# Kernel tuning notes

Hardware: AMD Instinct MI355X
Metric: run time of the kernel (lower is better)

Reference implementation:

```python
import jax, jax.numpy as jnp
import numpy as np
from jax import lax

DN = ('NCHW', 'OIHW', 'NCHW')
NUM_CODES = 8192


def _conv(x, w, b):
    # Conv2d(k=4, s=2, p=1)
    y = lax.conv_general_dilated(x, w, (2, 2), ((1, 1), (1, 1)), dimension_numbers=DN)
    return y + b[None, :, None, None]


def _convT(x, w, b):
    # ConvTranspose2d(k=4, s=2, p=1) as lhs-dilated conv; kernel already in equivalent OIHW layout
    y = lax.conv_general_dilated(x, w, (1, 1), ((2, 2), (2, 2)), lhs_dilation=(2, 2), dimension_numbers=DN)
    return y + b[None, :, None, None]


def _aff(x, s, b):
    # eval-mode BatchNorm folded to per-channel affine
    return x * s[None, :, None, None] + b[None, :, None, None]


def _forward(x, ew1, eb1, bn1s, bn1b, ew2, eb2, bn2s, bn2b, ew3, eb3, bn3s, bn3b, ew4, eb4, embed, cluster_size, dw1, db1, dbn1s, dbn1b, dw2, db2, dbn2s, dbn2b, dw3, db3, dbn3s, dbn3b, dw4, db4):
    sg = lax.stop_gradient
    embed = sg(embed)          # codebook is a torch buffer -> no grad
    cluster_size = sg(cluster_size)
    relu = jax.nn.relu
    # ---- Encoder: 4 stride-2 convs ----
    h = relu(_aff(_conv(x, ew1, eb1), bn1s, bn1b))
    h = relu(_aff(_conv(h, ew2, eb2), bn2s, bn2b))
    h = relu(_aff(_conv(h, ew3, eb3), bn3s, bn3b))
    z = _conv(h, ew4, eb4)                       # [B, D, G, G]
    zt = jnp.transpose(z, (0, 2, 3, 1))          # [B, G, G, D]
    D = zt.shape[-1]
    flat = zt.reshape(-1, D)                     # [N, D]
    N = flat.shape[0]
    # ---- VQ: pairwise squared distance + argmin codebook lookup ----
    dist = (flat * flat).sum(1, keepdims=True) - 2.0 * (flat @ embed.T) + (embed * embed).sum(1)[None, :]
    soft = jax.nn.softmax(-dist, axis=-1)        # temperature = 1.0
    codes = jnp.argmin(dist, axis=1)             # [N]
    zq = embed[codes]                            # [N, D]
    commitment_loss = jnp.mean((flat - sg(zq)) ** 2)
    codebook_loss = jnp.mean((zq - sg(flat)) ** 2)
    avg_soft = soft.mean(0)
    usage_entropy = -(avg_soft * jnp.log(avg_soft + 1e-10)).sum()
    diversity_loss = -usage_entropy / float(np.log(NUM_CODES))
    zq_st = flat + sg(zq - flat)                 # straight-through estimator
    zq_grid = jnp.transpose(zq_st.reshape(zt.shape), (0, 3, 1, 2))  # [B, D, G, G]
    # ---- Decoder: 4 stride-2 transposed convs ----
    h = relu(_aff(_convT(zq_grid, dw1, db1), dbn1s, dbn1b))
    h = relu(_aff(_convT(h, dw2, db2), dbn2s, dbn2b))
    h = relu(_aff(_convT(h, dw3, db3), dbn3s, dbn3b))
    recon = jax.nn.sigmoid(_convT(h, dw4, db4))
    recon_loss = jnp.mean((recon - x) ** 2)
    # ---- usage stats (no-grad in torch) ----
    hard_avg = jnp.zeros(NUM_CODES, flat.dtype).at[codes].add(1.0) / N
    perplexity = jnp.exp(-(hard_avg * jnp.log(hard_avg + 1e-10)).sum())
    active_codes = (cluster_size > 1).sum()
    codes_grid = codes.reshape(zt.shape[:-1])
    return (recon, recon_loss, codes_grid, zq_grid, commitment_loss, codebook_loss, diversity_loss, usage_entropy, perplexity, active_codes)


def setup_inputs() -> dict:
    keys = iter(jax.random.split(jax.random.key(0), 64))
    def randn(shape, s=1.0):
        return jax.random.normal(next(keys), shape, jnp.float32) * s
    def randu(shape):
        return jax.random.uniform(next(keys), shape, dtype=jnp.float32)
    B, H = 32, 256
    return {
        'x': randu((B, 1, H, H)),
        'ew1': randn((64, 1, 4, 4), 0.25), 'eb1': randn((64,), 0.1),
        'bn1s': randu((64,)), 'bn1b': randn((64,), 0.1),
        'ew2': randn((64, 64, 4, 4), 0.03), 'eb2': randn((64,), 0.1),
        'bn2s': randu((64,)), 'bn2b': randn((64,), 0.1),
        'ew3': randn((128, 64, 4, 4), 0.03), 'eb3': randn((128,), 0.1),
        'bn3s': randu((128,)), 'bn3b': randn((128,), 0.1),
        'ew4': randn((64, 128, 4, 4), 0.02), 'eb4': randn((64,), 0.1),
        'embed': randn((8192, 64), 0.5),
        'cluster_size': jnp.ones((8192,), jnp.float32),
        'dw1': randn((128, 64, 4, 4), 0.03), 'db1': randn((128,), 0.1),
        'dbn1s': randu((128,)), 'dbn1b': randn((128,), 0.1),
        'dw2': randn((64, 128, 4, 4), 0.02), 'db2': randn((64,), 0.1),
        'dbn2s': randu((64,)), 'dbn2b': randn((64,), 0.1),
        'dw3': randn((64, 64, 4, 4), 0.03), 'db3': randn((64,), 0.1),
        'dbn3s': randu((64,)), 'dbn3b': randn((64,), 0.1),
        'dw4': randn((1, 64, 4, 4), 0.03), 'db4': randn((1,), 0.1),
    }


def reference(x, ew1, eb1, bn1s, bn1b, ew2, eb2, bn2s, bn2b, ew3, eb3, bn3s, bn3b, ew4, eb4, embed, cluster_size, dw1, db1, dbn1s, dbn1b, dw2, db2, dbn2s, dbn2b, dw3, db3, dbn3s, dbn3b, dw4, db4):
    return _forward(x, ew1, eb1, bn1s, bn1b, ew2, eb2, bn2s, bn2b, ew3, eb3, bn3s, bn3b, ew4, eb4, embed, cluster_size, dw1, db1, dbn1s, dbn1b, dw2, db2, dbn2s, dbn2b, dw3, db3, dbn3s, dbn3b, dw4, db4)
```

## Files before the change

kernel.cpp:

```cpp
#include <hip/hip_runtime.h>
#include <cstdint>
#include <cstddef>


#define DEVI __device__ __forceinline__

typedef short  short8 __attribute__((ext_vector_type(8)));
typedef __bf16 bf16x8 __attribute__((ext_vector_type(8)));
typedef float  f32x16 __attribute__((ext_vector_type(16)));

DEVI f32x16 MFMA(bf16x8 a, bf16x8 b, f32x16 c){
  return __builtin_amdgcn_mfma_f32_32x32x16_bf16(a, b, c, 0, 0, 0);
}

DEVI ushort f2bf(float f){
  unsigned u = __float_as_uint(f);
  unsigned r = (u + 0x7FFFu + ((u >> 16) & 1u)) >> 16;
  return (ushort)r;
}
DEVI float bf2f(ushort h){ return __uint_as_float(((unsigned)h) << 16); }

union U8 { short8 s; bf16x8 b; };
DEVI bf16x8 ldg8u(const ushort* p){
  U8 u; u.s = *(const short8*)p; return u.b;
}

DEVI float wred64(float v){
  #pragma unroll
  for (int off=32; off>0; off>>=1) v += __shfl_down(v, off, 64);
  return v;
}

#define O_RECON     0
#define O_RLOSS     2097152
#define O_CODES     2097153
#define O_ZQ        2105345
#define O_COMMIT    2629633
#define O_CB        2629634
#define O_DIV       2629635
#define O_UE        2629636
#define O_PERP      2629637
#define O_ACT       2629638

#define WS_R1       0ull
#define A3H_OFF     0ull
#define A3M_OFF     8912896ull
#define A3L_OFF     17825792ull
#define PP_OFF      33554432ull
#define MT_OFF      37748736ull
#define PARTA_OFF   41943040ull
#define A2H_OFF     134217728ull
#define A2M_OFF     151519232ull
#define A2L_OFF     168820736ull
#define EH_OFF      134217728ull
#define EM_OFF      135266304ull
#define EL_OFF      136314880ull
#define FH_OFF      137363456ull
#define FM_OFF      138412032ull
#define FL_OFF      139460608ull
#define D2H_OFF     134217728ull
#define D2L_OFF     151519232ull
#define D1H_OFF     168820736ull
#define D1L_OFF     177733632ull
#define WS_FLAT     186646528ull
#define WS_ZQP      188743680ull
#define WS_WT       191102976ull
#define WT_E2       (WS_WT)
#define WT_E3       (WT_E2 + 393216ull)
#define WT_E4       (WT_E3 + 786432ull)
#define WT_D1       (WT_E4 + 786432ull)
#define WT_D2       (WT_D1 + 524288ull)
#define WT_D3       (WT_D2 + 524288ull)
#define WS_W4       (WT_D3 + 262144ull)
#define WS_STATS    (WS_W4 + 4096ull)
#define ST_RMP      (WS_STATS)
#define ST_CNT      (ST_RMP + 65536ull)
#define ST_AVGS     (ST_CNT + 32768ull)
#define ST_ROWZI    (ST_AVGS + 32768ull)
#define ST_CODESQ   (ST_ROWZI + 32768ull)
#define ST_LOSS     (ST_CODESQ + 32768ull)
#define ST_ROWM     (ST_LOSS + 32768ull)

DEVI void wsplit_body(int i, const float* src, ushort* dh, ushort* dm,
                      ushort* dl, int OC, int CIN, int isT, int three)
{
  if (i >= 16*OC*CIN) return;
  int cin = i % CIN; int t = i / CIN; int oc = t % OC; int tap = t / OC;
  int st;
  if (isT){
    int pq = tap>>2, ab = tap&3;
    int p = pq>>1, q = pq&1, a = ab>>1, b = ab&1;
    st = (p + 2*a)*4 + (q + 2*b);
  } else st = tap;
  float v = src[((size_t)oc*CIN + cin)*16 + st];
  ushort h = f2bf(v); float r = v - bf2f(h);
  if (three){
    ushort m = f2bf(r); float r2 = r - bf2f(m);
    dm[i] = m; dl[i] = f2bf(r2);
  } else {
    dl[i] = f2bf(r);
  }
  dh[i] = h;
}

DEVI void zpad_body(int i, unsigned* b0, unsigned* b1, unsigned* b2,
                    int rows, int Wp, int cwords)
{
  int total = rows*2*cwords;
  if (i >= total) return;
  int pos = i / cwords, cw = i % cwords;
  int row = pos >> 1, side = pos & 1;
  size_t w = ((size_t)row*Wp + (side ? (Wp-1) : 0))*cwords + cw;
  b0[w] = 0u;
  if (b1) b1[w] = 0u;
  if (b2) b2[w] = 0u;
}

__global__ __launch_bounds__(256) void k_prep(
    const float* __restrict__ ew2, const float* __restrict__ ew3,
    const float* __restrict__ ew4, const float* __restrict__ dw1,
    const float* __restrict__ dw2, const float* __restrict__ dw3,
    const float* __restrict__ dw4,
    ushort* wE2h, ushort* wE2m, ushort* wE2l,
    ushort* wE3h, ushort* wE3m, ushort* wE3l,
    ushort* wE4h, ushort* wE4m, ushort* wE4l,
    ushort* wD1h, ushort* wD1l, ushort* wD2h, ushort* wD2l,
    ushort* wD3h, ushort* wD3l, float* w4,
    unsigned* A2h, unsigned* A2m, unsigned* A2l,
    unsigned* zqPh, unsigned* zqPl,
    unsigned int* cnt, unsigned long long* rmp, float* loss)
{
  int b = blockIdx.x, tid = threadIdx.x;
  if (b < 32){
    int i = b*256 + tid;
    if (i < 8192){ cnt[i]=0u; rmp[i]=0xFFFFFFFFFFFFFFFFull; }
    if (i < 8) loss[i]=0.f;
  } else if (b < 288){
    wsplit_body((b-32)*256 + tid, ew2, wE2h, wE2m, wE2l, 64, 64, 0, 1);
  } else if (b < 800){
    wsplit_body((b-288)*256 + tid, ew3, wE3h, wE3m, wE3l, 128, 64, 0, 1);
  } else if (b < 1312){
    wsplit_body((b-800)*256 + tid, ew4, wE4h, wE4m, wE4l, 64, 128, 0, 1);
  } else if (b < 1824){
    wsplit_body((b-1312)*256 + tid, dw1, wD1h, nullptr, wD1l, 128, 64, 1, 0);
  } else if (b < 2336){
    wsplit_body((b-1824)*256 + tid, dw2, wD2h, nullptr, wD2l, 64, 128, 1, 0);
  } else if (b < 2592){
    wsplit_body((b-2336)*256 + tid, dw3, wD3h, nullptr, wD3l, 64, 64, 1, 0);
  } else if (b < 2596){
    int i = (b-2592)*256 + tid;
    if (i < 1024){
      int c = i & 63; int t16 = i >> 6;
      int pq = t16 >> 2, ab = t16 & 3;
      int p = pq>>1, q = pq&1, a = ab>>1, bb = ab&1;
      w4[i] = dw4[(size_t)c*16 + (p+2*a)*4 + (q+2*bb)];
    }
  } else if (b < 3108){
    zpad_body((b-2596)*256 + tid, A2h, A2m, A2l, 32*64, 66, 32);
  } else {
    zpad_body((b-3108)*256 + tid, zqPh, zqPl, nullptr, 32*16, 18, 32);
  }
}

__global__ __launch_bounds__(256) void k_zpadA3(unsigned* b0, unsigned* b1,
                                                unsigned* b2)
{
  zpad_body(blockIdx.x*256 + threadIdx.x, b0, b1, b2, 32*32, 34, 64);
}
__global__ __launch_bounds__(256) void k_zpadD(unsigned* d1h, unsigned* d1l,
                                               unsigned* d2h, unsigned* d2l)
{
  int b = blockIdx.x;
  if (b < 512) zpad_body(b*256 + threadIdx.x, d1h, d1l, nullptr, 32*32, 34, 64);
  else zpad_body((b-512)*256 + threadIdx.x, d2h, d2l, nullptr, 32*64, 66, 32);
}

__global__ __launch_bounds__(256) void k_esplit(
    const float* __restrict__ src, ushort* __restrict__ dh,
    ushort* __restrict__ dm, ushort* __restrict__ dl)
{
  int i = blockIdx.x*256 + threadIdx.x;
  float v = src[i];
  ushort h = f2bf(v); float r1 = v - bf2f(h);
  ushort m = f2bf(r1); float r2 = r1 - bf2f(m);
  dh[i] = h; dm[i] = m; dl[i] = f2bf(r2);
}

__global__ __launch_bounds__(256) void enc_conv1(
    const float* __restrict__ x, const float* __restrict__ w,
    const float* __restrict__ cb_, const float* __restrict__ bns,
    const float* __restrict__ bnb, float* __restrict__ out)
{
  __shared__ __align__(16) float sIn[34][36];
  __shared__ __align__(16) float sW[64][16];
  int b = blockIdx.x;
  int t = b & 63, n = b >> 6;
  int ty = t >> 3, tx = t & 7;
  int oy0 = ty*16, ox0 = tx*16;
  int iy0 = 2*oy0 - 1, ix0 = 2*ox0 - 1;
  int tid = threadIdx.x;
  int spg = tid & 31, og = tid >> 5;
  int sy = spg >> 1, x0 = (spg & 1)*8;

  if (tid < 64){
    const float* wp = w + tid*16;
    *(float4*)&sW[tid][0]  = *(const float4*)(wp);
    *(float4*)&sW[tid][4]  = *(const float4*)(wp+4);
    *(float4*)&sW[tid][8]  = *(const float4*)(wp+8);
    *(float4*)&sW[tid][12] = *(const float4*)(wp+12);
  }
  for (int e = tid; e < 34*34; e += 256){
    int rr = e/34, cc = e%34;
    int iy = iy0+rr, ix = ix0+cc;
    float v = 0.f;
    if ((unsigned)iy < 256u && (unsigned)ix < 256u)
      v = x[(size_t)n*65536 + iy*256 + ix];
    sIn[rr][cc] = v;
  }
  __syncthreads();

  float acc[8][8];
  #pragma unroll
  for (int j=0;j<8;j++)
    #pragma unroll
    for (int xi=0;xi<8;xi++) acc[j][xi]=0.f;

  #pragma unroll
  for (int ky=0; ky<4; ky++){
    int riy = 2*sy + ky;
    float seg[20];
    #pragma unroll
    for (int i=0;i<5;i++){
      float4 v = *(const float4*)&sIn[riy][2*x0 + 4*i];
      seg[4*i+0]=v.x; seg[4*i+1]=v.y; seg[4*i+2]=v.z; seg[4*i+3]=v.w;
    }
    #pragma unroll
    for (int j=0;j<8;j++){
      float4 w4v = *(const float4*)&sW[og*8+j][ky*4];
      #pragma unroll
      for (int xi=0; xi<8; xi++){
        acc[j][xi] = fmaf(seg[2*xi+0], w4v.x,
                     fmaf(seg[2*xi+1], w4v.y,
                     fmaf(seg[2*xi+2], w4v.z,
                     fmaf(seg[2*xi+3], w4v.w, acc[j][xi]))));
      }
    }
  }

  float sc[8], sh[8];
  #pragma unroll
  for (int j=0;j<8;j++){
    int oc = og*8+j;
    sc[j] = bns[oc];
    sh[j] = fmaf(cb_[oc], sc[j], bnb[oc]);
  }
  int oy = oy0 + sy;
  #pragma unroll
  for (int xi=0; xi<8; xi++){
    int oxg = ox0 + x0 + xi;
    float* op = out + (((size_t)n*128 + oy)*128 + oxg)*64 + og*8;
    float4 q0, q1;
    q0.x = fmaxf(fmaf(acc[0][xi], sc[0], sh[0]), 0.f);
    q0.y = fmaxf(fmaf(acc[1][xi], sc[1], sh[1]), 0.f);
    q0.z = fmaxf(fmaf(acc[2][xi], sc[2], sh[2]), 0.f);
    q0.w = fmaxf(fmaf(acc[3][xi], sc[3], sh[3]), 0.f);
    q1.x = fmaxf(fmaf(acc[4][xi], sc[4], sh[4]), 0.f);
    q1.y = fmaxf(fmaf(acc[5][xi], sc[5], sh[5]), 0.f);
    q1.z = fmaxf(fmaf(acc[6][xi], sc[6], sh[6]), 0.f);
    q1.w = fmaxf(fmaf(acc[7][xi], sc[7], sh[7]), 0.f);
    *(float4*)op     = q0;
    *(float4*)(op+4) = q1;
  }
}

template<int CIN, int OC, int OUTW, int OUTH, int INW, int INH, bool XPAD,
         int INMODE, int OUTMODE>
__global__ __launch_bounds__(256) void enc_conv(
    const float* __restrict__ in,
    const ushort* __restrict__ aH, const ushort* __restrict__ aM,
    const ushort* __restrict__ aL,
    const ushort* __restrict__ wtH, const ushort* __restrict__ wtM,
    const ushort* __restrict__ wtL,
    const float* __restrict__ cb_, const float* __restrict__ bns,
    const float* __restrict__ bnb,
    float* __restrict__ outF,
    ushort* __restrict__ oH, ushort* __restrict__ oM, ushort* __restrict__ oL,
    int nOcg)
{
  constexpr int INWP  = (INMODE==1) ? (INW+2) : (XPAD ? (INW+2) : INW);
  constexpr int WP    = INW + 2;
  constexpr int NROWS = 64 / OUTW;
  constexpr int AELEM = NROWS * WP * CIN;
  constexpr int BCIN  = (CIN > 64) ? 64 : CIN;
  constexpr int BELEM = 64 * BCIN;
  constexpr int NCH   = CIN / BCIN;
  constexpr int NSTG  = 16 * NCH;
  constexpr int PFI   = BELEM / 8 / 256;
  constexpr int SCRSZ = (3*BELEM*2 > 64*68*4) ? 3*BELEM*2 : 64*68*4;

  __shared__ __align__(16) ushort sAh[AELEM], sAm[AELEM], sAl[AELEM];
  __shared__ __align__(16) char sScr[SCRSZ];
  ushort* sBh = (ushort*)sScr;
  ushort* sBm = sBh + BELEM;
  ushort* sBl = sBm + BELEM;
  float*  sC  = (float*)sScr;

  int b = blockIdx.x;
  int ocg = b % nOcg; b /= nOcg;
  int yb  = b % (OUTH/NROWS); b /= (OUTH/NROWS);
  int n = b;
  int oy0 = yb * NROWS, oc0 = ocg * 64;

  int tid = threadIdx.x;
  int l = tid & 63, wave = tid >> 6;
  int wm = wave >> 1, wn = wave & 1;
  int r = l & 31, kp = l >> 5;
  int idx = wm*32 + r;
  int oy_off = idx / OUTW, ox = idx % OUTW;

  int pfoc[PFI], pfc8[PFI];
  #pragma unroll
  for (int it=0; it<PFI; it++){
    int c = tid + it*256;
    pfoc[it] = c / (BCIN/8);
    pfc8[it] = (c % (BCIN/8)) * 8;
  }
  short8 pf0[PFI], pf1[PFI], pf2[PFI];
  {
    #pragma unroll
    for (int it=0; it<PFI; it++){
      size_t off = ((size_t)oc0 + pfoc[it])*CIN + pfc8[it];
      pf0[it] = *(const short8*)(wtH + off);
      pf1[it] = *(const short8*)(wtM + off);
      pf2[it] = *(const short8*)(wtL + off);
    }
  }

  f32x16 acc0, acc1, acc2, acc3;
  #pragma unroll
  for (int i=0;i<16;i++){ acc0[i]=0.f; acc1[i]=0.f; acc2[i]=0.f; acc3[i]=0.f; }

  const size_t nbase = (size_t)n * INH * INWP * CIN;
  int sidx = 0;

  for (int ky = 0; ky < 4; ky++){
    __syncthreads();
    for (int c = tid; c < AELEM/8; c += 256){
      int j  = c / (WP*CIN/8);
      int rm = c % (WP*CIN/8);
      int lx = rm / (CIN/8);
      int c8 = (rm % (CIN/8)) * 8;
      int iy = 2*(oy0 + j) - 1 + ky;
      bool ok = (unsigned)iy < (unsigned)INH;
      unsigned off = (unsigned)(((j*WP + lx)*CIN + c8)*2) ^ ((((unsigned)lx>>1)&15u)<<4);
      if constexpr (INMODE == 0){
        int gx = XPAD ? lx : (lx - 1);
        if (!XPAD) ok = ok && ((unsigned)gx < (unsigned)INW);
        float4 v0 = {0,0,0,0}, v1 = {0,0,0,0};
        if (ok){
          const float* s = in + nbase + ((size_t)iy*INWP + gx)*CIN + c8;
          v0 = *(const float4*)s; v1 = *(const float4*)(s+4);
        }
        float vv[8] = {v0.x,v0.y,v0.z,v0.w,v1.x,v1.y,v1.z,v1.w};
        short8 hh, mm, ll;
        #pragma unroll
        for (int e=0;e<8;e++){
          ushort h = f2bf(vv[e]); float r1 = vv[e] - bf2f(h);
          ushort m = f2bf(r1);    float r2 = r1 - bf2f(m);
          hh[e] = (short)h; mm[e] = (short)m; ll[e] = (short)f2bf(r2);
        }
        *(short8*)((char*)sAh + off) = hh;
        *(short8*)((char*)sAm + off) = mm;
        *(short8*)((char*)sAl + off) = ll;
      } else {
        short8 vh = {0,0,0,0,0,0,0,0}, vm = vh, vl = vh;
        if (ok){
          size_t s = nbase + ((size_t)iy*INWP + lx)*CIN + c8;
          vh = *(const short8*)(aH + s);
          vm = *(const short8*)(aM + s);
          vl = *(const short8*)(aL + s);
        }
        *(short8*)((char*)sAh + off) = vh;
        *(short8*)((char*)sAm + off) = vm;
        *(short8*)((char*)sAl + off) = vl;
      }
    }
    for (int kx = 0; kx < 4; kx++){
      for (int chi = 0; chi < NCH; chi++){
        int ch = chi * BCIN;
        __syncthreads();
        #pragma unroll
        for (int it=0; it<PFI; it++){
          unsigned off = (unsigned)((pfoc[it]*BCIN + pfc8[it])*2)
                         ^ (((unsigned)pfoc[it]&15u)<<4);
          *(short8*)((char*)sBh + off) = pf0[it];
          *(short8*)((char*)sBm + off) = pf1[it];
          *(short8*)((char*)sBl + off) = pf2[it];
        }
        __syncthreads();
        if (sidx + 1 < NSTG){
          int ns = sidx + 1;
          int ntap = ns / NCH, nchi = ns % NCH;
          #pragma unroll
          for (int it=0; it<PFI; it++){
            size_t off = ((size_t)ntap*OC + oc0 + pfoc[it])*CIN
                         + nchi*BCIN + pfc8[it];
            pf0[it] = *(const short8*)(wtH + off);
            pf1[it] = *(const short8*)(wtM + off);
            pf2[it] = *(const short8*)(wtL + off);
          }
        }
        sidx++;
        int lx = 2*ox + kx;
        unsigned asw  = ((((unsigned)lx>>1)&15u)<<4);
        unsigned alin = (unsigned)(((oy_off*WP + lx)*CIN)*2);
        int ocl = wn*32 + r;
        unsigned bsw  = (((unsigned)ocl&15u)<<4);
        unsigned blin = (unsigned)((ocl*BCIN)*2);
        #pragma unroll
        for (int ct = 0; ct < BCIN/16; ct++){
          unsigned kbA = (unsigned)((ch + ct*16 + kp*8)*2);
          unsigned kbB = (unsigned)((ct*16 + kp*8)*2);
          unsigned ao = (alin + kbA) ^ asw;
          unsigned bo = (blin + kbB) ^ bsw;
          bf16x8 ah = *(const bf16x8*)((char*)sAh + ao);
          bf16x8 am = *(const bf16x8*)((char*)sAm + ao);
          bf16x8 al = *(const bf16x8*)((char*)sAl + ao);
          bf16x8 bh = *(const bf16x8*)((char*)sBh + bo);
          bf16x8 bm = *(const bf16x8*)((char*)sBm + bo);
          bf16x8 bl = *(const bf16x8*)((char*)sBl + bo);
          acc0 = MFMA(ah, bh, acc0);
          acc1 = MFMA(ah, bm, acc1);
          acc2 = MFMA(am, bh, acc2);
          acc3 = MFMA(ah, bl, acc3);
          acc0 = MFMA(am, bm, acc0);
          acc1 = MFMA(al, bh, acc1);
        }
      }
    }
  }
  __syncthreads();
  #pragma unroll
  for (int q = 0; q < 16; q++){
    int rowt = (q&3) + 8*(q>>2) + 4*kp;
    sC[(wm*32 + rowt)*68 + wn*32 + r] = (acc0[q] + acc1[q]) + (acc2[q] + acc3[q]);
  }
  __syncthreads();
  {
    int m = tid >> 2, qq = tid & 3;
    int oc = oc0 + qq*16;
    int oyg = oy0 + m / OUTW;
    int oxg = m % OUTW;
    if constexpr (OUTMODE == 1){
      size_t row = (size_t)n*256 + oyg*16 + oxg;
      float* op = outF + row*64 + qq*16;
      size_t pb = row*64 + qq*16;
      short8 hv[2], mv[2], lv[2];
      #pragma unroll
      for (int i=0;i<16;i++){
        float v = sC[m*68 + qq*16 + i] + cb_[oc+i];
        op[i] = v;
        ushort h = f2bf(v); float r1 = v - bf2f(h);
        ushort mm = f2bf(r1); float r2 = r1 - bf2f(mm);
        hv[i>>3][i&7]=(short)h; mv[i>>3][i&7]=(short)mm; lv[i>>3][i&7]=(short)f2bf(r2);
      }
      *(short8*)(oH + pb) = hv[0]; *(short8*)(oH + pb + 8) = hv[1];
      *(short8*)(oM + pb) = mv[0]; *(short8*)(oM + pb + 8) = mv[1];
      *(short8*)(oL + pb) = lv[0]; *(short8*)(oL + pb + 8) = lv[1];
    } else {
      size_t pbase = (((size_t)n*OUTH + oyg)*(OUTW+2) + oxg + 1)*OC + oc;
      short8 hv[2], mv[2], lv[2];
      #pragma unroll
      for (int i=0;i<16;i++){
        float s1 = bns[oc+i];
        float s2 = fmaf(cb_[oc+i], s1, bnb[oc+i]);
        float v = fmaxf(fmaf(sC[m*68 + qq*16 + i], s1, s2), 0.f);
        ushort h = f2bf(v); float r1 = v - bf2f(h);
        ushort mm = f2bf(r1); float r2 = r1 - bf2f(mm);
        hv[i>>3][i&7]=(short)h; mv[i>>3][i&7]=(short)mm; lv[i>>3][i&7]=(short)f2bf(r2);
      }
      *(short8*)(oH + pbase)   = hv[0]; *(short8*)(oH + pbase+8) = hv[1];
      *(short8*)(oM + pbase)   = mv[0]; *(short8*)(oM + pbase+8) = mv[1];
      *(short8*)(oL + pbase)   = lv[0]; *(short8*)(oL + pbase+8) = lv[1];
    }
  }
}

__global__ __launch_bounds__(256) void k_codesq(const float* __restrict__ embed,
                                                float* __restrict__ codesq)
{
  int j = blockIdx.x*4 + (threadIdx.x>>6);
  int c = threadIdx.x & 63;
  float e = embed[(size_t)j*64 + c];
  float s = wred64(e*e);
  if (c==0) codesq[j] = s;
}

DEVI float rmp_minval(unsigned long long v){
  unsigned skey = (unsigned)(v >> 32);
  unsigned u = (skey & 0x80000000u) ? (skey ^ 0x80000000u) : ~skey;
  return __uint_as_float(u);
}

__global__ __launch_bounds__(256) void vq_min(
    const ushort* __restrict__ fH, const ushort* __restrict__ fM,
    const ushort* __restrict__ fL,
    const ushort* __restrict__ eH, const ushort* __restrict__ eM,
    const ushort* __restrict__ eL,
    const float* __restrict__ codesq,
    unsigned long long* __restrict__ rmp,
    float* __restrict__ Pp, float* __restrict__ Mt)
{
  __shared__ __align__(16) ushort sAh[128*64], sAm[128*64], sAl[128*64];
  int cblk = blockIdx.x & 63, fblk = blockIdx.x >> 6;
  int code0 = cblk*128, f0 = fblk*128;
  int tid = threadIdx.x, l = tid&63, wave = tid>>6;
  int wm = wave>>1, wn = wave&1, r = l&31, kp = l>>5;

  for (int c = tid; c < 1024; c += 256){
    int rr = c >> 3, c8 = (c & 7)*8;
    size_t s = (size_t)(code0+rr)*64 + c8;
    unsigned off = (unsigned)((rr*64 + c8)*2) ^ (((unsigned)rr&15u)<<4);
    *(short8*)((char*)sAh + off) = *(const short8*)(eH + s);
    *(short8*)((char*)sAm + off) = *(const short8*)(eM + s);
    *(short8*)((char*)sAl + off) = *(const short8*)(eL + s);
  }
  __syncthreads();

  f32x16 acc[2][2];
  #pragma unroll
  for (int mt=0;mt<2;mt++)
    #pragma unroll
    for (int nt=0;nt<2;nt++)
      #pragma unroll
      for (int i=0;i<16;i++) acc[mt][nt][i]=0.f;

  #pragma unroll
  for (int ks=0; ks<4; ks++){
    unsigned kb = (unsigned)((ks*16 + kp*8)*2);
    int ko = ks*16 + kp*8;
    bf16x8 Ah[2],Am[2],Al[2],Bh[2],Bm[2],Bl[2];
    #pragma unroll
    for (int mt=0;mt<2;mt++){
      int rowi = wm*64 + mt*32 + r;
      unsigned o = ((unsigned)(rowi*128) + kb) ^ (((unsigned)rowi&15u)<<4);
      Ah[mt] = *(const bf16x8*)((char*)sAh + o);
      Am[mt] = *(const bf16x8*)((char*)sAm + o);
      Al[mt] = *(const bf16x8*)((char*)sAl + o);
    }
    #pragma unroll
    for (int nt=0;nt<2;nt++){
      int coli = f0 + wn*64 + nt*32 + r;
      size_t bo = (size_t)coli*64 + ko;
      Bh[nt] = ldg8u(fH + bo);
      Bm[nt] = ldg8u(fM + bo);
      Bl[nt] = ldg8u(fL + bo);
    }
    #pragma unroll
    for (int mt=0;mt<2;mt++)
      #pragma unroll
      for (int nt=0;nt<2;nt++){
        acc[mt][nt] = MFMA(Ah[mt], Bh[nt], acc[mt][nt]);
        acc[mt][nt] = MFMA(Ah[mt], Bm[nt], acc[mt][nt]);
        acc[mt][nt] = MFMA(Am[mt], Bh[nt], acc[mt][nt]);
        acc[mt][nt] = MFMA(Ah[mt], Bl[nt], acc[mt][nt]);
        acc[mt][nt] = MFMA(Am[mt], Bm[nt], acc[mt][nt]);
        acc[mt][nt] = MFMA(Al[mt], Bh[nt], acc[mt][nt]);
      }
  }

  float cqv[2][16];
  #pragma unroll
  for (int mt=0; mt<2; mt++)
    #pragma unroll
    for (int g=0; g<4; g++){
      float4 cv = *(const float4*)(codesq + code0 + wm*64 + mt*32 + 8*g + 4*kp);
      cqv[mt][4*g+0]=cv.x; cqv[mt][4*g+1]=cv.y;
      cqv[mt][4*g+2]=cv.z; cqv[mt][4*g+3]=cv.w;
    }

  #pragma unroll
  for (int nt=0; nt<2; nt++){
    int col = f0 + wn*64 + nt*32 + r;
    unsigned long long kmin = 0xFFFFFFFFFFFFFFFFull;
    #pragma unroll
    for (int mt=0; mt<2; mt++)
      #pragma unroll
      for (int q=0; q<16; q++){
        float d = cqv[mt][q] - 2.f*acc[mt][nt][q];
        int code = code0 + wm*64 + mt*32 + (q&3) + 8*(q>>2) + 4*kp;
        unsigned u = __float_as_uint(d);
        unsigned sgn = (unsigned)((int)u >> 31);
        unsigned skey = u ^ (sgn | 0x80000000u);
        unsigned long long key = (((unsigned long long)skey)<<32) | (unsigned)code;
        if (key < kmin) kmin = key;
      }
    unsigned long long o2 = __shfl_xor(kmin, 32, 64);
    if (o2 < kmin) kmin = o2;
    float mloc = rmp_minval(kmin);
    float p = 0.f;
    #pragma unroll
    for (int mt=0; mt<2; mt++)
      #pragma unroll
      for (int q=0; q<16; q++){
        float d = cqv[mt][q] - 2.f*acc[mt][nt][q];
        p += __expf(mloc - d);
      }
    p += __shfl_xor(p, 32, 64);
    if (kp == 0){
      atomicMin(&rmp[col], kmin);
      size_t pidx = (size_t)col*128 + (size_t)cblk*2 + wm;
      Pp[pidx] = p;
      Mt[pidx] = mloc;
    }
  }
}

__global__ __launch_bounds__(256) void k_rowz2(
    const unsigned long long* __restrict__ rmp,
    const float* __restrict__ Pp, const float* __restrict__ Mt,
    float* __restrict__ rowzi, float* __restrict__ rowm)
{
  int row = blockIdx.x*256 + threadIdx.x;
  float mg = rmp_minval(rmp[row]);
  const float* pp = Pp + (size_t)row*128;
  const float* mt = Mt + (size_t)row*128;
  float z = 0.f;
  for (int t = 0; t < 128; t++)
    z = fmaf(__expf(mg - mt[t]), pp[t], z);
  rowzi[row] = 1.f / z;
  rowm[row] = mg;
}

__global__ __launch_bounds__(256) void vq_avg(
    const ushort* __restrict__ fH, const ushort* __restrict__ fM,
    const ushort* __restrict__ fL,
    const ushort* __restrict__ eH, const ushort* __restrict__ eM,
    const ushort* __restrict__ eL,
    const float* __restrict__ codesq,
    const float* __restrict__ rowm,
    const float* __restrict__ rowzi,
    float* __restrict__ partA)
{
  __shared__ __align__(16) ushort sAh[128*64], sAm[128*64], sAl[128*64];
  __shared__ float colbuf[128];
  int cb = blockIdx.x & 63, rb = blockIdx.x >> 6;
  int row0 = rb*128, c0 = cb*128;
  int tid = threadIdx.x, l = tid&63, wave = tid>>6;
  int wm = wave>>1, wn = wave&1, r = l&31, kp = l>>5;

  if (tid < 128) colbuf[tid] = 0.f;

  for (int c = tid; c < 1024; c += 256){
    int rr = c >> 3, c8 = (c & 7)*8;
    size_t s = (size_t)(row0+rr)*64 + c8;
    unsigned off = (unsigned)((rr*64 + c8)*2) ^ (((unsigned)rr&15u)<<4);
    *(short8*)((char*)sAh + off) = *(const short8*)(fH + s);
    *(short8*)((char*)sAm + off) = *(const short8*)(fM + s);
    *(short8*)((char*)sAl + off) = *(const short8*)(fL + s);
  }
  __syncthreads();

  f32x16 acc[2][2];
  #pragma unroll
  for (int mt=0;mt<2;mt++)
    #pragma unroll
    for (int nt=0;nt<2;nt++)
      #pragma unroll
      for (int i=0;i<16;i++) acc[mt][nt][i]=0.f;

  #pragma unroll
  for (int ks=0; ks<4; ks++){
    unsigned kb = (unsigned)((ks*16 + kp*8)*2);
    int ko = ks*16 + kp*8;
    bf16x8 Ah[2],Am[2],Al[2],Bh[2],Bm[2],Bl[2];
    #pragma unroll
    for (int mt=0;mt<2;mt++){
      int rowi = wm*64 + mt*32 + r;
      unsigned o = ((unsigned)(rowi*128) + kb) ^ (((unsigned)rowi&15u)<<4);
      Ah[mt] = *(const bf16x8*)((char*)sAh + o);
      Am[mt] = *(const bf16x8*)((char*)sAm + o);
      Al[mt] = *(const bf16x8*)((char*)sAl + o);
    }
    #pragma unroll
    for (int nt=0;nt<2;nt++){
      int coli = c0 + wn*64 + nt*32 + r;
      size_t bo = (size_t)coli*64 + ko;
      Bh[nt] = ldg8u(eH + bo);
      Bm[nt] = ldg8u(eM + bo);
      Bl[nt] = ldg8u(eL + bo);
    }
    #pragma unroll
    for (int mt=0;mt<2;mt++)
      #pragma unroll
      for (int nt=0;nt<2;nt++){
        acc[mt][nt] = MFMA(Ah[mt], Bh[nt], acc[mt][nt]);
        acc[mt][nt] = MFMA(Ah[mt], Bm[nt], acc[mt][nt]);
        acc[mt][nt] = MFMA(Am[mt], Bh[nt], acc[mt][nt]);
        acc[mt][nt] = MFMA(Ah[mt], Bl[nt], acc[mt][nt]);
        acc[mt][nt] = MFMA(Am[mt], Bm[nt], acc[mt][nt]);
        acc[mt][nt] = MFMA(Al[mt], Bh[nt], acc[mt][nt]);
      }
  }

  float cq[2];
  cq[0] = codesq[c0 + wn*64 + r];
  cq[1] = codesq[c0 + wn*64 + 32 + r];
  float colacc[2] = {0.f, 0.f};
  #pragma unroll
  for (int mt=0; mt<2; mt++){
    #pragma unroll
    for (int q=0; q<16; q++){
      int rowt = (q&3) + 8*(q>>2) + 4*kp;
      int grow = row0 + wm*64 + mt*32 + rowt;
      float mi = rowm[grow];
      float zi = rowzi[grow];
      #pragma unroll
      for (int nt=0; nt<2; nt++){
        float d = cq[nt] - 2.f*acc[mt][nt][q];
        colacc[nt] = fmaf(__expf(mi - d), zi, colacc[nt]);
      }
    }
  }
  #pragma unroll
  for (int nt=0; nt<2; nt++){
    float o = __shfl_xor(colacc[nt], 32, 64);
    colacc[nt] += o;
    if (l < 32) atomicAdd(&colbuf[wn*64 + nt*32 + r], colacc[nt]);
  }
  __syncthreads();
  if (tid < 128)
    partA[(size_t)rb*8192 + c0 + tid] = colbuf[tid];
}

__global__ __launch_bounds__(256) void k_avgred(const float* __restrict__ partA,
                                                float* __restrict__ avgs)
{
  int j = blockIdx.x*256 + threadIdx.x;
  float s = 0.f;
  for (int rb = 0; rb < 64; rb++)
    s += partA[(size_t)rb*8192 + j];
  avgs[j] = s;
}

__global__ __launch_bounds__(256) void vq_post(
    const float* __restrict__ flat, const float* __restrict__ embed,
    const unsigned long long* __restrict__ rmp,
    float* __restrict__ out_codes, float* __restrict__ out_zq,
    ushort* __restrict__ zqPh, ushort* __restrict__ zqPl,
    float* __restrict__ loss, unsigned int* __restrict__ cnt)
{
  int r = blockIdx.x*4 + (threadIdx.x>>6);
  int c = threadIdx.x & 63;
  unsigned j = (unsigned)(rmp[r] & 0xFFFFFFFFull);
  float e = embed[(size_t)j*64 + c];
  float f = flat[(size_t)r*64 + c];
  int n = r>>8, rem = r&255, gy = rem>>4, gx = rem&15;
  out_zq[(((size_t)n*64 + c)*16 + gy)*16 + gx] = e;
  ushort h = f2bf(e);
  size_t pz = (((size_t)n*16 + gy)*18 + gx + 1)*64 + c;
  zqPh[pz] = h; zqPl[pz] = f2bf(e - bf2f(h));
  float d = f - e;
  float s2 = wred64(d*d);
  if (c==0){
    out_codes[r] = (float)j;
    atomicAdd(cnt + j, 1u);
    atomicAdd(loss + 1, s2);
  }
}

template<int CIN, int OC, int SW, int SH, bool OUTPAD, int OMODE, int NPAR>
__global__ __launch_bounds__(256) void dec_convT_m(
    const ushort* __restrict__ inH, const ushort* __restrict__ inL,
    const ushort* __restrict__ wtH, const ushort* __restrict__ wtL,
    const float* __restrict__ db, const float* __restrict__ bns,
    const float* __restrict__ bnb,
    ushort* __restrict__ oH, ushort* __restrict__ oL, int nOcg)
{
  constexpr int TR    = 64 / SW;
  constexpr int NRA   = TR + ((NPAR==4) ? 2 : 1);
  constexpr int WPin  = SW + 2;
  constexpr int AELEM = NRA * WPin * CIN;
  constexpr int OUTH  = 2*SH;
  constexpr int OW    = OUTPAD ? (2*SW+2) : (2*SW);

  __shared__ __align__(16) ushort sAh[AELEM], sAl[AELEM];

  int b = blockIdx.x;
  int p_blk = 0;
  if (NPAR == 2){ p_blk = b & 1; b >>= 1; }
  int ocg = b % nOcg; b /= nOcg;
  int tb = b % (SH/TR); b /= (SH/TR);
  int n = b;
  int t0 = tb * TR, oc0 = ocg * 64;
  const int ROWBASE = (NPAR==4) ? -1 : (p_blk - 1);

  int tid = threadIdx.x, l = tid&63, wave = tid>>6;
  int wm = wave>>1, wn = wave&1;
  int r = l&31, kp = l>>5;
  int idx = wm*32 + r;
  int t_off = idx / SW, s = idx % SW;
  int ocl = oc0 + wn*32 + r;

  float bn_s1 = bns[ocl];
  float bn_s2 = fmaf(db[ocl], bn_s1, bnb[ocl]);

  for (int c = tid; c < AELEM/8; c += 256){
    int j  = c / (WPin*CIN/8);
    int rm = c % (WPin*CIN/8);
    int lx = rm / (CIN/8);
    int c8 = (rm % (CIN/8)) * 8;
    int giy = t0 + ROWBASE + j;
    bool ok = (unsigned)giy < (unsigned)SH;
    short8 vh = {0,0,0,0,0,0,0,0}, vl = {0,0,0,0,0,0,0,0};
    if (ok){
      size_t sidx = (((size_t)n*SH + giy)*WPin + lx)*CIN + c8;
      vh = *(const short8*)(inH + sidx);
      vl = *(const short8*)(inL + sidx);
    }
    unsigned off = (unsigned)(((j*WPin + lx)*CIN + c8)*2) ^ (((unsigned)lx&15u)<<4);
    *(short8*)((char*)sAh + off) = vh;
    *(short8*)((char*)sAl + off) = vl;
  }
  __syncthreads();

  for (int pr = 0; pr < NPAR; pr++){
    int p2 = (NPAR==4) ? (pr>>1) : p_blk;
    int q2 = (NPAR==4) ? (pr&1)  : pr;
    int par = p2*2 + q2;

    f32x16 acc0, acc1, acc2;
    #pragma unroll
    for (int i=0;i<16;i++){ acc0[i]=0.f; acc1[i]=0.f; acc2[i]=0.f; }

    for (int ab = 0; ab < 4; ab++){
      int a = ab>>1, bb = ab&1;
      int rs = t_off + ((NPAR==4) ? (p2 + a) : a);
      int lx = s + q2 + bb;
      unsigned asw  = (((unsigned)lx&15u)<<4);
      unsigned alin = (unsigned)(((rs*WPin + lx)*CIN)*2);
      size_t brow = ((size_t)(par*4 + ab)*OC + ocl)*CIN;
      #pragma unroll
      for (int ct = 0; ct < CIN/16; ct++){
        int ko = ct*16 + kp*8;
        unsigned ao = (alin + (unsigned)(ko*2)) ^ asw;
        bf16x8 ah = *(const bf16x8*)((char*)sAh + ao);
        bf16x8 al = *(const bf16x8*)((char*)sAl + ao);
        bf16x8 bh = ldg8u(wtH + brow + ko);
        bf16x8 bl = ldg8u(wtL + brow + ko);
        acc0 = MFMA(ah, bh, acc0);
        acc1 = MFMA(ah, bl, acc1);
        acc2 = MFMA(al, bh, acc2);
      }
    }

    #pragma unroll
    for (int q = 0; q < 16; q++){
      int rowt = (q&3) + 8*(q>>2) + 4*kp;
      int m = wm*32 + rowt;
      int y  = 2*(t0 + m/SW) + p2;
      int xs = m % SW;
      int xp = OUTPAD ? (2*xs + q2 + 1) : (2*xs + q2);
      size_t base = (((size_t)n*OUTH + y)*OW + xp)*OC + ocl;
      float v = fmaxf(fmaf(acc0[q] + acc1[q] + acc2[q], bn_s1, bn_s2), 0.f);
      ushort h = f2bf(v);
      oH[base] = h;
      if constexpr (OMODE == 0){
        oL[base] = f2bf(v - bf2f(h));
      }
    }
  }
}

__global__ __launch_bounds__(256) void dec_convT4(
    const ushort* __restrict__ d3, const float* __restrict__ w4,
    const float* __restrict__ db4, const float* __restrict__ xref,
    float* __restrict__ recon, float* __restrict__ loss)
{
  __shared__ __align__(16) float sT[10*10*68];
  __shared__ __align__(16) float sWt[16*64];
  __shared__ float red[4];
  int b = blockIdx.x;
  int t = b & 255, n = b >> 8;
  int ty = t >> 4, tx = t & 15;
  int y0 = ty*16, x0 = tx*16;
  int r0 = y0/2 - 1, c0 = x0/2 - 1;
  int tid = threadIdx.x;

  *(float4*)&sWt[tid*4] = *(const float4*)(w4 + tid*4);

  const ushort* base = d3 + (size_t)n*128*128*64;
  for (int e = tid; e < 800; e += 256){
    int rr = e/80; int rem = e%80; int cc = rem/8; int c8 = (rem%8)*8;
    int gr = r0+rr, gc = c0+cc;
    short8 v = {0,0,0,0,0,0,0,0};
    if ((unsigned)gr<128u && (unsigned)gc<128u)
      v = *(const short8*)(base + ((size_t)gr*128+gc)*64 + c8);
    float* dst = &sT[(rr*10+cc)*68 + c8];
    float4 f0, f1;
    f0.x = bf2f((ushort)v[0]); f0.y = bf2f((ushort)v[1]);
    f0.z = bf2f((ushort)v[2]); f0.w = bf2f((ushort)v[3]);
    f1.x = bf2f((ushort)v[4]); f1.y = bf2f((ushort)v[5]);
    f1.z = bf2f((ushort)v[6]); f1.w = bf2f((ushort)v[7]);
    *(float4*)dst     = f0;
    *(float4*)(dst+4) = f1;
  }
  __syncthreads();

  int sy = tid>>4, sx = tid&15;
  int p = sy&1, q = sx&1;
  int lr0 = (sy>>1)+p, lc0 = (sx>>1)+q;
  int par = p*2+q;
  float4 a4 = {0,0,0,0};
  #pragma unroll
  for (int a=0;a<2;a++){
    #pragma unroll
    for (int bb=0;bb<2;bb++){
      const float* ip = &sT[((lr0+a)*10 + lc0+bb)*68];
      const float* wp = &sWt[(par*4+a*2+bb)*64];
      #pragma unroll
      for (int c=0;c<64;c+=4){
        float4 v  = *(const float4*)(ip+c);
        float4 wv = *(const float4*)(wp+c);
        a4.x = fmaf(v.x, wv.x, a4.x);
        a4.y = fmaf(v.y, wv.y, a4.y);
        a4.z = fmaf(v.z, wv.z, a4.z);
        a4.w = fmaf(v.w, wv.w, a4.w);
      }
    }
  }
  float acc = (a4.x + a4.y) + (a4.z + a4.w);
  float v = acc + db4[0];
  float rcn = 1.f/(1.f + __expf(-v));
  int y = y0+sy, x = x0+sx;
  size_t oi = (size_t)n*65536 + (size_t)y*256 + x;
  recon[oi] = rcn;
  float d = rcn - xref[oi];
  float s2 = wred64(d*d);
  if ((tid & 63)==0) red[tid>>6] = s2;
  __syncthreads();
  if (tid==0) atomicAdd(loss + 0, red[0]+red[1]+red[2]+red[3]);
}

__global__ __launch_bounds__(256) void k_final(
    const float* __restrict__ avgs, const unsigned int* __restrict__ cnt,
    const float* __restrict__ cluster, const float* __restrict__ loss,
    float* __restrict__ dout)
{
  __shared__ float red[3][4];
  int tid = threadIdx.x;
  float e1=0.f, e2=0.f, ac=0.f;
  for (int j=tid; j<8192; j+=256){
    float a = avgs[j] * (1.f/8192.f);
    e1 += a * __logf(a + 1e-10f);
    float h = (float)cnt[j] * (1.f/8192.f);
    e2 += h * __logf(h + 1e-10f);
    ac += (cluster[j] > 1.f) ? 1.f : 0.f;
  }
  e1 = wred64(e1); e2 = wred64(e2); ac = wred64(ac);
  int wv = tid >> 6;
  if ((tid & 63)==0){ red[0][wv]=e1; red[1][wv]=e2; red[2][wv]=ac; }
  __syncthreads();
  if (tid==0){
    float s1 = red[0][0]+red[0][1]+red[0][2]+red[0][3];
    float s2 = red[1][0]+red[1][1]+red[1][2]+red[1][3];
    float s3 = red[2][0]+red[2][1]+red[2][2]+red[2][3];
    float ue = -s1;
    dout[O_RLOSS]  = loss[0] * (1.f/2097152.f);
    float cc = loss[1] * (1.f/524288.f);
    dout[O_COMMIT] = cc;
    dout[O_CB]     = cc;
    dout[O_DIV]    = -ue / 9.010913347279288f;
    dout[O_UE]     = ue;
    dout[O_PERP]   = __expf(-s2);
    dout[O_ACT]    = s3;
  }
}

extern "C" void kernel_launch(void* const* d_in, const int* in_sizes, int n_in,
                              void* d_out, int out_size, void* d_ws, size_t ws_size,
                              hipStream_t stream)
{
  (void)in_sizes; (void)n_in; (void)out_size; (void)ws_size;
  const float* x     = (const float*)d_in[0];
  const float* ew1   = (const float*)d_in[1];
  const float* eb1   = (const float*)d_in[2];
  const float* bn1s  = (const float*)d_in[3];
  const float* bn1b  = (const float*)d_in[4];
  const float* ew2   = (const float*)d_in[5];
  const float* eb2   = (const float*)d_in[6];
  const float* bn2s  = (const float*)d_in[7];
  const float* bn2b  = (const float*)d_in[8];
  const float* ew3   = (const float*)d_in[9];
  const float* eb3   = (const float*)d_in[10];
  const float* bn3s  = (const float*)d_in[11];
  const float* bn3b  = (const float*)d_in[12];
  const float* ew4   = (const float*)d_in[13];
  const float* eb4   = (const float*)d_in[14];
  const float* embed = (const float*)d_in[15];
  const float* clsz  = (const float*)d_in[16];
  const float* dw1   = (const float*)d_in[17];
  const float* db1   = (const float*)d_in[18];
  const float* dbn1s = (const float*)d_in[19];
  const float* dbn1b = (const float*)d_in[20];
  const float* dw2   = (const float*)d_in[21];
  const float* db2   = (const float*)d_in[22];
  const float* dbn2s = (const float*)d_in[23];
  const float* dbn2b = (const float*)d_in[24];
  const float* dw3   = (const float*)d_in[25];
  const float* db3   = (const float*)d_in[26];
  const float* dbn3s = (const float*)d_in[27];
  const float* dbn3b = (const float*)d_in[28];
  const float* dw4   = (const float*)d_in[29];
  const float* db4   = (const float*)d_in[30];

  float* out = (float*)d_out;
  uint8_t* wsb = (uint8_t*)d_ws;

  float*  A1   = (float*)(wsb + WS_R1);
  ushort* D3b  = (ushort*)(wsb + WS_R1);
  ushort* A3h  = (ushort*)(wsb + A3H_OFF);
  ushort* A3m  = (ushort*)(wsb + A3M_OFF);
  ushort* A3l  = (ushort*)(wsb + A3L_OFF);
  float*  Pp   = (float*)(wsb + PP_OFF);
  float*  Mt   = (float*)(wsb + MT_OFF);
  float*  partA= (float*)(wsb + PARTA_OFF);
  ushort* A2h  = (ushort*)(wsb + A2H_OFF);
  ushort* A2m  = (ushort*)(wsb + A2M_OFF);
  ushort* A2l  = (ushort*)(wsb + A2L_OFF);
  ushort* eH   = (ushort*)(wsb + EH_OFF);
  ushort* eM   = (ushort*)(wsb + EM_OFF);
  ushort* eL   = (ushort*)(wsb + EL_OFF);
  ushort* fH   = (ushort*)(wsb + FH_OFF);
  ushort* fM   = (ushort*)(wsb + FM_OFF);
  ushort* fL   = (ushort*)(wsb + FL_OFF);
  ushort* D1h  = (ushort*)(wsb + D1H_OFF);
  ushort* D1l  = (ushort*)(wsb + D1L_OFF);
  ushort* D2h  = (ushort*)(wsb + D2H_OFF);
  ushort* D2l  = (ushort*)(wsb + D2L_OFF);
  float*  flat = (float*)(wsb + WS_FLAT);
  ushort* zqPh = (ushort*)(wsb + WS_ZQP);
  ushort* zqPl = (ushort*)(wsb + WS_ZQP + 1179648ull);

  ushort* wE2h = (ushort*)(wsb + WT_E2);
  ushort* wE2m = wE2h + 65536;  ushort* wE2l = wE2m + 65536;
  ushort* wE3h = (ushort*)(wsb + WT_E3);
  ushort* wE3m = wE3h + 131072; ushort* wE3l = wE3m + 131072;
  ushort* wE4h = (ushort*)(wsb + WT_E4);
  ushort* wE4m = wE4h + 131072; ushort* wE4l = wE4m + 131072;
  ushort* wD1h = (ushort*)(wsb + WT_D1);
  ushort* wD1l = wD1h + 131072;
  ushort* wD2h = (ushort*)(wsb + WT_D2);
  ushort* wD2l = wD2h + 131072;
  ushort* wD3h = (ushort*)(wsb + WT_D3);
  ushort* wD3l = wD3h + 65536;
  float*  w4   = (float*)(wsb + WS_W4);

  unsigned long long* rmp = (unsigned long long*)(wsb + ST_RMP);
  unsigned int* cnt = (unsigned int*)(wsb + ST_CNT);
  float* avgs   = (float*)(wsb + ST_AVGS);
  float* rowzi  = (float*)(wsb + ST_ROWZI);
  float* codesq = (float*)(wsb + ST_CODESQ);
  float* loss   = (float*)(wsb + ST_LOSS);
  float* rowm   = (float*)(wsb + ST_ROWM);

  dim3 B(256);

  k_prep<<<3236, B, 0, stream>>>(
      ew2, ew3, ew4, dw1, dw2, dw3, dw4,
      wE2h, wE2m, wE2l, wE3h, wE3m, wE3l, wE4h, wE4m, wE4l,
      wD1h, wD1l, wD2h, wD2l, wD3h, wD3l, w4,
      (unsigned*)A2h, (unsigned*)A2m, (unsigned*)A2l,
      (unsigned*)zqPh, (unsigned*)zqPl,
      cnt, rmp, loss);

  enc_conv1<<<2048, B, 0, stream>>>(x, ew1, eb1, bn1s, bn1b, A1);
  enc_conv<64,64,64,64,128,128,false,0,0><<<2048, B, 0, stream>>>(
      A1, nullptr, nullptr, nullptr, wE2h, wE2m, wE2l, eb2, bn2s, bn2b,
      nullptr, A2h, A2m, A2l, 1);
  k_zpadA3<<<512, B, 0, stream>>>((unsigned*)A3h, (unsigned*)A3m, (unsigned*)A3l);
  enc_conv<64,128,32,32,64,64,true,1,0><<<1024, B, 0, stream>>>(
      nullptr, A2h, A2m, A2l, wE3h, wE3m, wE3l, eb3, bn3s, bn3b,
      nullptr, A3h, A3m, A3l, 2);
  k_esplit<<<2048, B, 0, stream>>>(embed, eH, eM, eL);
  enc_conv<128,64,16,16,32,32,true,1,1><<<128, B, 0, stream>>>(
      nullptr, A3h, A3m, A3l, wE4h, wE4m, wE4l, eb4, eb4, eb4,
      flat, fH, fM, fL, 1);

  k_codesq<<<2048, B, 0, stream>>>(embed, codesq);

  vq_min<<<4096, B, 0, stream>>>(fH, fM, fL, eH, eM, eL, codesq, rmp, Pp, Mt);
  k_rowz2<<<32, B, 0, stream>>>(rmp, Pp, Mt, rowzi, rowm);
  vq_avg<<<4096, B, 0, stream>>>(fH, fM, fL, eH, eM, eL, codesq, rowm, rowzi, partA);
  k_avgred<<<32, B, 0, stream>>>(partA, avgs);

  vq_post<<<2048, B, 0, stream>>>(flat, embed, rmp, out + O_CODES, out + O_ZQ,
                                  zqPh, zqPl, loss, cnt);

  k_zpadD<<<1024, B, 0, stream>>>((unsigned*)D1h, (unsigned*)D1l,
                                  (unsigned*)D2h, (unsigned*)D2l);

  dec_convT_m<64,128,16,16,true,0,4><<<256, B, 0, stream>>>(
      zqPh, zqPl, wD1h, wD1l, db1, dbn1s, dbn1b, D1h, D1l, 2);
  dec_convT_m<128,64,32,32,true,0,2><<<1024, B, 0, stream>>>(
      D1h, D1l, wD2h, wD2l, db2, dbn2s, dbn2b, D2h, D2l, 1);
  dec_convT_m<64,64,64,64,false,2,4><<<2048, B, 0, stream>>>(
      D2h, D2l, wD3h, wD3l, db3, dbn3s, dbn3b, D3b, nullptr, 1);
  dec_convT4<<<8192, B, 0, stream>>>(D3b, w4, db4, x, out + O_RECON, loss);

  k_final<<<1, B, 0, stream>>>(avgs, cnt, clsz, loss, out);
}
```

Before: 912.6 us.

## Merge small prep kernels and write conv epilogue directly from accumulators

Folds the embed split and codebook-norm kernels into one launch, and moves the decoder zero-padding into vq_post as extra blocks, removing two kernel launches. The encoder conv epilogue now writes results straight from MFMA accumulator registers instead of staging them through shared memory. That drops two barriers and the aliased scratch buffer, but it replaces the vectorized 16-byte stores with scattered 2- and 4-byte stores. The B tiles now get their own shared memory, which may raise LDS usage.

```diff
diff --git a/kernel.cpp b/kernel.cpp
--- a/kernel.cpp
+++ b/kernel.cpp
@@ -167,23 +167,26 @@
 {
   zpad_body(blockIdx.x*256 + threadIdx.x, b0, b1, b2, 32*32, 34, 64);
 }
-__global__ __launch_bounds__(256) void k_zpadD(unsigned* d1h, unsigned* d1l,
-                                               unsigned* d2h, unsigned* d2l)
+
+__global__ __launch_bounds__(256) void k_eprep(
+    const float* __restrict__ embed,
+    ushort* __restrict__ dh, ushort* __restrict__ dm, ushort* __restrict__ dl,
+    float* __restrict__ codesq)
 {
   int b = blockIdx.x;
-  if (b < 512) zpad_body(b*256 + threadIdx.x, d1h, d1l, nullptr, 32*32, 34, 64);
-  else zpad_body((b-512)*256 + threadIdx.x, d2h, d2l, nullptr, 32*64, 66, 32);
-}
-
-__global__ __launch_bounds__(256) void k_esplit(
-    const float* __restrict__ src, ushort* __restrict__ dh,
-    ushort* __restrict__ dm, ushort* __restrict__ dl)
-{
-  int i = blockIdx.x*256 + threadIdx.x;
-  float v = src[i];
-  ushort h = f2bf(v); float r1 = v - bf2f(h);
-  ushort m = f2bf(r1); float r2 = r1 - bf2f(m);
-  dh[i] = h; dm[i] = m; dl[i] = f2bf(r2);
+  if (b < 2048){
+    int i = b*256 + threadIdx.x;
+    float v = embed[i];
+    ushort h = f2bf(v); float r1 = v - bf2f(h);
+    ushort m = f2bf(r1); float r2 = r1 - bf2f(m);
+    dh[i] = h; dm[i] = m; dl[i] = f2bf(r2);
+  } else {
+    int j = (b-2048)*4 + (threadIdx.x>>6);
+    int c = threadIdx.x & 63;
+    float e = embed[(size_t)j*64 + c];
+    float s = wred64(e*e);
+    if (c==0) codesq[j] = s;
+  }
 }
 
 __global__ __launch_bounds__(256) void enc_conv1(
@@ -296,14 +299,9 @@
   constexpr int NCH   = CIN / BCIN;
   constexpr int NSTG  = 16 * NCH;
   constexpr int PFI   = BELEM / 8 / 256;
-  constexpr int SCRSZ = (3*BELEM*2 > 64*68*4) ? 3*BELEM*2 : 64*68*4;
 
   __shared__ __align__(16) ushort sAh[AELEM], sAm[AELEM], sAl[AELEM];
-  __shared__ __align__(16) char sScr[SCRSZ];
-  ushort* sBh = (ushort*)sScr;
-  ushort* sBm = sBh + BELEM;
-  ushort* sBl = sBm + BELEM;
-  float*  sC  = (float*)sScr;
+  __shared__ __align__(16) ushort sBh[BELEM], sBm[BELEM], sBl[BELEM];
 
   int b = blockIdx.x;
   int ocg = b % nOcg; b /= nOcg;
@@ -439,61 +437,44 @@
       }
     }
   }
-  __syncthreads();
-  #pragma unroll
-  for (int q = 0; q < 16; q++){
-    int rowt = (q&3) + 8*(q>>2) + 4*kp;
-    sC[(wm*32 + rowt)*68 + wn*32 + r] = (acc0[q] + acc1[q]) + (acc2[q] + acc3[q]);
-  }
-  __syncthreads();
   {
-    int m = tid >> 2, qq = tid & 3;
-    int oc = oc0 + qq*16;
-    int oyg = oy0 + m / OUTW;
-    int oxg = m % OUTW;
+    int oce = oc0 + wn*32 + r;
     if constexpr (OUTMODE == 1){
-      size_t row = (size_t)n*256 + oyg*16 + oxg;
-      float* op = outF + row*64 + qq*16;
-      size_t pb = row*64 + qq*16;
-      short8 hv[2], mv[2], lv[2];
-      #pragma unroll
-      for (int i=0;i<16;i++){
-        float v = sC[m*68 + qq*16 + i] + cb_[oc+i];
-        op[i] = v;
+      float cbv = cb_[oce];
+      #pragma unroll
+      for (int q = 0; q < 16; q++){
+        int rowt = (q&3) + 8*(q>>2) + 4*kp;
+        int m = wm*32 + rowt;
+        int oyg = oy0 + m / OUTW;
+        int oxg = m % OUTW;
+        size_t row = (size_t)n*256 + oyg*16 + oxg;
+        float v = (acc0[q] + acc1[q]) + (acc2[q] + acc3[q]) + cbv;
+        outF[row*64 + oce] = v;
         ushort h = f2bf(v); float r1 = v - bf2f(h);
         ushort mm = f2bf(r1); float r2 = r1 - bf2f(mm);
-        hv[i>>3][i&7]=(short)h; mv[i>>3][i&7]=(short)mm; lv[i>>3][i&7]=(short)f2bf(r2);
-      }
-      *(short8*)(oH + pb) = hv[0]; *(short8*)(oH + pb + 8) = hv[1];
-      *(short8*)(oM + pb) = mv[0]; *(short8*)(oM + pb + 8) = mv[1];
-      *(short8*)(oL + pb) = lv[0]; *(short8*)(oL + pb + 8) = lv[1];
+        oH[row*64 + oce] = h;
+        oM[row*64 + oce] = mm;
+        oL[row*64 + oce] = f2bf(r2);
+      }
     } else {
-      size_t pbase = (((size_t)n*OUTH + oyg)*(OUTW+2) + oxg + 1)*OC + oc;
-      short8 hv[2], mv[2], lv[2];
-      #pragma unroll
-      for (int i=0;i<16;i++){
-        float s1 = bns[oc+i];
-        float s2 = fmaf(cb_[oc+i], s1, bnb[oc+i]);
-        float v = fmaxf(fmaf(sC[m*68 + qq*16 + i], s1, s2), 0.f);
+      float s1 = bns[oce];
+      float s2 = fmaf(cb_[oce], s1, bnb[oce]);
+      #pragma unroll
+      for (int q = 0; q < 16; q++){
+        int rowt = (q&3) + 8*(q>>2) + 4*kp;
+        int m = wm*32 + rowt;
+        int oyg = oy0 + m / OUTW;
+        int oxg = m % OUTW;
+        size_t pbase = (((size_t)n*OUTH + oyg)*(OUTW+2) + oxg + 1)*OC + oce;
+        float v = fmaxf(fmaf((acc0[q] + acc1[q]) + (acc2[q] + acc3[q]), s1, s2), 0.f);
         ushort h = f2bf(v); float r1 = v - bf2f(h);
         ushort mm = f2bf(r1); float r2 = r1 - bf2f(mm);
-        hv[i>>3][i&7]=(short)h; mv[i>>3][i&7]=(short)mm; lv[i>>3][i&7]=(short)f2bf(r2);
-      }
-      *(short8*)(oH + pbase)   = hv[0]; *(short8*)(oH + pbase+8) = hv[1];
-      *(short8*)(oM + pbase)   = mv[0]; *(short8*)(oM + pbase+8) = mv[1];
-      *(short8*)(oL + pbase)   = lv[0]; *(short8*)(oL + pbase+8) = lv[1];
-    }
-  }
-}
-
-__global__ __launch_bounds__(256) void k_codesq(const float* __restrict__ embed,
-                                                float* __restrict__ codesq)
-{
-  int j = blockIdx.x*4 + (threadIdx.x>>6);
-  int c = threadIdx.x & 63;
-  float e = embed[(size_t)j*64 + c];
-  float s = wred64(e*e);
-  if (c==0) codesq[j] = s;
+        oH[pbase] = h;
+        oM[pbase] = mm;
+        oL[pbase] = f2bf(r2);
+      }
+    }
+  }
 }
 
 DEVI float rmp_minval(unsigned long long v){
@@ -748,9 +729,18 @@
     const unsigned long long* __restrict__ rmp,
     float* __restrict__ out_codes, float* __restrict__ out_zq,
     ushort* __restrict__ zqPh, ushort* __restrict__ zqPl,
-    float* __restrict__ loss, unsigned int* __restrict__ cnt)
-{
-  int r = blockIdx.x*4 + (threadIdx.x>>6);
+    float* __restrict__ loss, unsigned int* __restrict__ cnt,
+    unsigned* __restrict__ d1h, unsigned* __restrict__ d1l,
+    unsigned* __restrict__ d2h, unsigned* __restrict__ d2l)
+{
+  int blk = blockIdx.x;
+  if (blk >= 2048){
+    int zb = blk - 2048;
+    if (zb < 512) zpad_body(zb*256 + threadIdx.x, d1h, d1l, nullptr, 32*32, 34, 64);
+    else zpad_body((zb-512)*256 + threadIdx.x, d2h, d2l, nullptr, 32*64, 66, 32);
+    return;
+  }
+  int r = blk*4 + (threadIdx.x>>6);
   int c = threadIdx.x & 63;
   unsigned j = (unsigned)(rmp[r] & 0xFFFFFFFFull);
   float e = embed[(size_t)j*64 + c];
@@ -1082,22 +1072,19 @@
   enc_conv<64,128,32,32,64,64,true,1,0><<<1024, B, 0, stream>>>(
       nullptr, A2h, A2m, A2l, wE3h, wE3m, wE3l, eb3, bn3s, bn3b,
       nullptr, A3h, A3m, A3l, 2);
-  k_esplit<<<2048, B, 0, stream>>>(embed, eH, eM, eL);
+  k_eprep<<<4096, B, 0, stream>>>(embed, eH, eM, eL, codesq);
   enc_conv<128,64,16,16,32,32,true,1,1><<<128, B, 0, stream>>>(
       nullptr, A3h, A3m, A3l, wE4h, wE4m, wE4l, eb4, eb4, eb4,
       flat, fH, fM, fL, 1);
-
-  k_codesq<<<2048, B, 0, stream>>>(embed, codesq);
 
   vq_min<<<4096, B, 0, stream>>>(fH, fM, fL, eH, eM, eL, codesq, rmp, Pp, Mt);
   k_rowz2<<<32, B, 0, stream>>>(rmp, Pp, Mt, rowzi, rowm);
   vq_avg<<<4096, B, 0, stream>>>(fH, fM, fL, eH, eM, eL, codesq, rowm, rowzi, partA);
   k_avgred<<<32, B, 0, stream>>>(partA, avgs);
 
-  vq_post<<<2048, B, 0, stream>>>(flat, embed, rmp, out + O_CODES, out + O_ZQ,
-                                  zqPh, zqPl, loss, cnt);
-
-  k_zpadD<<<1024, B, 0, stream>>>((unsigned*)D1h, (unsigned*)D1l,
+  vq_post<<<3072, B, 0, stream>>>(flat, embed, rmp, out + O_CODES, out + O_ZQ,
+                                  zqPh, zqPl, loss, cnt,
+                                  (unsigned*)D1h, (unsigned*)D1l,
                                   (unsigned*)D2h, (unsigned*)D2l);
 
   dec_convT_m<64,128,16,16,true,0,4><<<256, B, 0, stream>>>(
```

Measured after the change: 906.4 us (median of 3 runs). About the same (-0.7%).
